# Kernel optimization log

Measured on AMD Instinct MI355X. Metric: run time of the kernel, lower is better.

The kernel has to match this reference:

```python
import jax, jax.numpy as jnp
import numpy as np

K_CONST = 0.005
D_U = 0.001
D_V = 0.005
LAYERS = [3, 256, 256, 256, 256, 2]
N_PTS = 131072


def setup_inputs() -> dict:
    key = jax.random.key(0)
    ks = jax.random.split(key, 3 + 2 * (len(LAYERS) - 1))
    inp = {
        "t": jax.random.uniform(ks[0], (N_PTS, 1), dtype=jnp.float32),
        "x": jax.random.uniform(ks[1], (N_PTS, 1), dtype=jnp.float32),
        "y": jax.random.uniform(ks[2], (N_PTS, 1), dtype=jnp.float32),
    }
    # PyTorch nn.Linear default init: U(-1/sqrt(fan_in), 1/sqrt(fan_in))
    for i in range(len(LAYERS) - 1):
        fan_in = LAYERS[i]
        s = 1.0 / np.sqrt(fan_in)
        inp[f"W{i}"] = jax.random.uniform(ks[3 + 2 * i], (LAYERS[i], LAYERS[i + 1]),
                                          minval=-s, maxval=s, dtype=jnp.float32)
        inp[f"b{i}"] = jax.random.uniform(ks[4 + 2 * i], (LAYERS[i + 1],),
                                          minval=-s, maxval=s, dtype=jnp.float32)
    return inp


def _mlp(params, inp):
    # inp: (3,) -> (2,) tanh MLP (tanh on all but last layer)
    h = inp
    for W, b in params[:-1]:
        h = jnp.tanh(h @ W + b)
    W, b = params[-1]
    return h @ W + b


def reference(t, x, y, W0, b0, W1, b1, W2, b2, W3, b3, W4, b4):
    params = [(W0, b0), (W1, b1), (W2, b2), (W3, b3), (W4, b4)]
    net = lambda p: _mlp(params, p)  # (3,) -> (2,)

    pts = jnp.concatenate([t, x, y], axis=1)            # (N, 3)
    uv = jax.vmap(net)(pts)                              # (N, 2)
    jac = jax.vmap(jax.jacrev(net))(pts)                 # (N, 2, 3)
    hess = jax.vmap(jax.jacfwd(jax.jacrev(net)))(pts)    # (N, 2, 3, 3)

    u = uv[:, 0:1]
    v = uv[:, 1:2]
    u_t = jac[:, 0, 0:1]
    v_t = jac[:, 1, 0:1]
    u_xx = hess[:, 0, 1, 1][:, None]
    u_yy = hess[:, 0, 2, 2][:, None]
    v_xx = hess[:, 1, 1, 1][:, None]
    v_yy = hess[:, 1, 2, 2][:, None]

    f = u - u ** 3 - K_CONST - v + D_U * (u_xx + u_yy) - u_t
    g = u - v + D_V * (v_xx + v_yy) - v_t
    return (u, v, f, g)
```

## Files before the change

kernel.cpp:

```cpp
#include <hip/hip_runtime.h>
#include <math.h>

#define N_PTS   131072
#define K_CONST 0.005f
#define D_U     0.001f
#define D_V     0.005f

typedef unsigned short u16;
typedef unsigned int   u32;
typedef __attribute__((ext_vector_type(8))) _Float16 f16x8;
typedef __attribute__((ext_vector_type(4))) float    f32x4;
typedef __attribute__((ext_vector_type(4))) u16      u16x4;
typedef __attribute__((ext_vector_type(8))) u16      u16x8;
typedef __attribute__((ext_vector_type(2))) u32      u32x2;
typedef __attribute__((ext_vector_type(4))) u32      u32x4;

__device__ __forceinline__ u16 f2h(float x){
    _Float16 h = (_Float16)x;
    return __builtin_bit_cast(u16, h);
}
__device__ __forceinline__ float h2f(u16 h){
    return (float)__builtin_bit_cast(_Float16, h);
}
__device__ __forceinline__ u32 pkrtz(float a, float b){
    return __builtin_bit_cast(u32, __builtin_amdgcn_cvt_pkrtz(a, b));
}
__device__ __forceinline__ u32x2 pk4(float a, float b, float c, float d){
    u32x2 r;
    r.x = pkrtz(a, b);
    r.y = pkrtz(c, d);
    return r;
}
__device__ __forceinline__ u32x4 pk8(const float* v){
    u32x4 r;
    r.x = pkrtz(v[0], v[1]);
    r.y = pkrtz(v[2], v[3]);
    r.z = pkrtz(v[4], v[5]);
    r.w = pkrtz(v[6], v[7]);
    return r;
}

__device__ __forceinline__ float tanh_fast(float z){
    float e = __expf(2.f * z);
    return 1.f - 2.f * __builtin_amdgcn_rcpf(e + 1.f);
}

__global__ void prep_weights(const float* __restrict__ W1, const float* __restrict__ W2,
                             const float* __restrict__ W3, u16* __restrict__ ws)
{
    int gid  = blockIdx.x * 256 + threadIdx.x;
    int lane = gid & 63;
    int nt   = (gid >> 6) & 15;
    int ks   = (gid >> 10) & 7;
    int L    = gid >> 13;
    if (L >= 3) return;
    const float* W = (L == 0) ? W1 : ((L == 1) ? W2 : W3);
    int n  = nt * 16 + (lane & 15);
    int kg = lane >> 4;
    u16 h[8];
    #pragma unroll
    for (int j = 0; j < 8; ++j) {
        int k = ks * 32 + kg * 8 + j;
        h[j] = f2h(W[k * 256 + n]);
    }
    size_t ostore = ((size_t)((L * 16 + nt) * 8 + ks) * 64 + lane) * 8;
    *(u16x8*)&ws[ostore] = *(u16x8*)h;
}


#define KSTEP(KS, WC, WN, P0, P1)                                                          \
  {                                                                                        \
    WN[0] = *(const f16x8*)(P0);                                                           \
    WN[1] = *(const f16x8*)(P1);                                                           \
    int hoff = mbase + ((64 * (KS) + 16 * kg) ^ mxor);                                     \
    f16x8 hv = *(const f16x8*)(Hb + 0 * 8192 + hoff);                                      \
    f16x8 ht = *(const f16x8*)(Hb + 1 * 8192 + hoff);                                      \
    f16x8 hx = *(const f16x8*)(Hb + 2 * 8192 + hoff);                                      \
    f16x8 hy = *(const f16x8*)(Hb + 3 * 8192 + hoff);                                      \
    f16x8 hl = *(const f16x8*)(Hb + 4 * 8192 + hoff);                                      \
    __builtin_amdgcn_s_setprio(1);                                                         \
    _Pragma("unroll")                                                                      \
    for (int nt = 0; nt < 2; ++nt) {                                                       \
      acc[0][nt] = __builtin_amdgcn_mfma_f32_16x16x32_f16(WC[nt], hv, acc[0][nt], 0, 0, 0);\
      acc[1][nt] = __builtin_amdgcn_mfma_f32_16x16x32_f16(WC[nt], ht, acc[1][nt], 0, 0, 0);\
      acc[2][nt] = __builtin_amdgcn_mfma_f32_16x16x32_f16(WC[nt], hx, acc[2][nt], 0, 0, 0);\
      acc[3][nt] = __builtin_amdgcn_mfma_f32_16x16x32_f16(WC[nt], hy, acc[3][nt], 0, 0, 0);\
      acc[4][nt] = __builtin_amdgcn_mfma_f32_16x16x32_f16(WC[nt], hl, acc[4][nt], 0, 0, 0);\
    }                                                                                      \
    __builtin_amdgcn_s_setprio(0);                                                         \
  }

__global__ __launch_bounds__(512, 4)
void pinn_mfma6(const float* __restrict__ t_in, const float* __restrict__ x_in,
                const float* __restrict__ y_in,
                const float* __restrict__ W0, const float* __restrict__ b0,
                const float* __restrict__ b1, const float* __restrict__ b2,
                const float* __restrict__ b3,
                const float* __restrict__ W4, const float* __restrict__ b4,
                const u16* __restrict__ ws,
                float* __restrict__ out)
{
    __shared__ u16 H[5 * 16 * 256];
    char* Hb = (char*)H;

    const int tid  = threadIdx.x;
    const int lane = tid & 63;
    const int wv   = tid >> 6;

    {
        int p = tid & 15, c = tid >> 4;
        int g0 = blockIdx.x * 16 + p;
        float tv = t_in[g0], xv = x_in[g0], yv = y_in[g0];
        int n0 = c * 8;
        float w0[8], w1[8], w2[8], bb[8];
        #pragma unroll
        for (int q = 0; q < 2; ++q) {
            *(float4*)&w0[q*4] = *(const float4*)&W0[0*256 + n0 + q*4];
            *(float4*)&w1[q*4] = *(const float4*)&W0[1*256 + n0 + q*4];
            *(float4*)&w2[q*4] = *(const float4*)&W0[2*256 + n0 + q*4];
            *(float4*)&bb[q*4] = *(const float4*)&b0[n0 + q*4];
        }
        float sv[8], st[8], sx[8], sy[8], sl[8];
        #pragma unroll
        for (int j = 0; j < 8; ++j) {
            float z = tv*w0[j] + xv*w1[j] + yv*w2[j] + bb[j];
            float a = tanh_fast(z);
            float g = 1.f - a*a;
            sv[j] = a;
            st[j] = g * w0[j];
            sx[j] = g * w1[j];
            sy[j] = g * w2[j];
            sl[j] = -2.f * a * g * (w1[j]*w1[j] + w2[j]*w2[j]);
        }
        int off = p * 512 + ((2 * n0) ^ (p << 4));
        *(u32x4*)(Hb + 0*8192 + off) = pk8(sv);
        *(u32x4*)(Hb + 1*8192 + off) = pk8(st);
        *(u32x4*)(Hb + 2*8192 + off) = pk8(sx);
        *(u32x4*)(Hb + 3*8192 + off) = pk8(sy);
        *(u32x4*)(Hb + 4*8192 + off) = pk8(sl);
    }
    __syncthreads();

    const int mrow  = lane & 15;
    const int kg    = lane >> 4;
    const int mxor  = mrow << 4;
    const int mbase = mrow * 512;

    const u16* pW0 = ws + (size_t)(wv * 2) * 4096 + lane * 8;
    const u16* pW1 = pW0 + 4096;

    f16x8 whA[2], whB[2];
    whA[0] = *(const f16x8*)(pW0);
    whA[1] = *(const f16x8*)(pW1);

    #pragma unroll 1
    for (int L = 0; L < 3; ++L) {
        const float* bL = (L == 0) ? b1 : ((L == 1) ? b2 : b3);

        f32x4 acc[5][2];
        #pragma unroll
        for (int s = 0; s < 5; ++s) {
            acc[s][0] = (f32x4){0.f, 0.f, 0.f, 0.f};
            acc[s][1] = (f32x4){0.f, 0.f, 0.f, 0.f};
        }

        const u16* pL0 = pW0 + L * 65536;
        const u16* pL1 = pW1 + L * 65536;
        const int  Ln  = (L < 2) ? (L + 1) : 2;
        const u16* pN0 = pW0 + Ln * 65536;
        const u16* pN1 = pW1 + Ln * 65536;

        KSTEP(0, whA, whB, pL0 + 1*512, pL1 + 1*512);
        KSTEP(1, whB, whA, pL0 + 2*512, pL1 + 2*512);
        KSTEP(2, whA, whB, pL0 + 3*512, pL1 + 3*512);
        KSTEP(3, whB, whA, pL0 + 4*512, pL1 + 4*512);
        KSTEP(4, whA, whB, pL0 + 5*512, pL1 + 5*512);
        KSTEP(5, whB, whA, pL0 + 6*512, pL1 + 6*512);
        KSTEP(6, whA, whB, pL0 + 7*512, pL1 + 7*512);
        KSTEP(7, whB, whA, pN0, pN1);

        __syncthreads();

        #pragma unroll
        for (int nt = 0; nt < 2; ++nt) {
            int nb = (wv * 2 + nt) * 16 + kg * 4;
            float4 bv = *(const float4*)&bL[nb];
            float bva[4] = {bv.x, bv.y, bv.z, bv.w};
            float oa[4], ot[4], ox[4], oy[4], ol[4];
            #pragma unroll
            for (int r = 0; r < 4; ++r) {
                float z0 = acc[0][nt][r] + bva[r];
                float a  = tanh_fast(z0);
                float g  = 1.f - a * a;
                float zt = acc[1][nt][r];
                float zx = acc[2][nt][r];
                float zy = acc[3][nt][r];
                float zl = acc[4][nt][r];
                oa[r] = a;
                ot[r] = g * zt;
                ox[r] = g * zx;
                oy[r] = g * zy;
                ol[r] = g * zl - 2.f * a * g * (zx*zx + zy*zy);
            }
            int off = mbase + ((2 * nb) ^ mxor);
            *(u32x2*)(Hb + 0*8192 + off) = pk4(oa[0], oa[1], oa[2], oa[3]);
            *(u32x2*)(Hb + 1*8192 + off) = pk4(ot[0], ot[1], ot[2], ot[3]);
            *(u32x2*)(Hb + 2*8192 + off) = pk4(ox[0], ox[1], ox[2], ox[3]);
            *(u32x2*)(Hb + 3*8192 + off) = pk4(oy[0], oy[1], oy[2], oy[3]);
            *(u32x2*)(Hb + 4*8192 + off) = pk4(ol[0], ol[1], ol[2], ol[3]);
        }
        __syncthreads();
    }

    {
        int p = tid >> 5, i = tid & 31;
        int k0 = i * 8;
        int off = p * 512 + ((2 * k0) ^ (p << 4));
        u16x8 hv = *(const u16x8*)(Hb + 0*8192 + off);
        u16x8 ht = *(const u16x8*)(Hb + 1*8192 + off);
        u16x8 hl = *(const u16x8*)(Hb + 4*8192 + off);
        float w4[16];
        #pragma unroll
        for (int q = 0; q < 4; ++q)
            *(float4*)&w4[q*4] = *(const float4*)&W4[k0 * 2 + q * 4];
        float pu = 0.f, pv = 0.f, put = 0.f, pvt = 0.f, plu = 0.f, plv = 0.f;
        #pragma unroll
        for (int j = 0; j < 8; ++j) {
            float vv = h2f(hv[j]);
            float tt = h2f(ht[j]);
            float ll = h2f(hl[j]);
            float wa = w4[2*j], wb2 = w4[2*j + 1];
            pu  += vv * wa;  pv  += vv * wb2;
            put += tt * wa;  pvt += tt * wb2;
            plu += ll * wa;  plv += ll * wb2;
        }
        #pragma unroll
        for (int m = 1; m < 32; m <<= 1) {
            pu  += __shfl_xor(pu, m);   pv  += __shfl_xor(pv, m);
            put += __shfl_xor(put, m);  pvt += __shfl_xor(pvt, m);
            plu += __shfl_xor(plu, m);  plv += __shfl_xor(plv, m);
        }
        if (i == 0) {
            float u = pu + b4[0];
            float v = pv + b4[1];
            int gpt = blockIdx.x * 16 + p;
            float fo = u - u*u*u - K_CONST - v + D_U * plu - put;
            float go = u - v + D_V * plv - pvt;
            out[0 * N_PTS + gpt] = u;
            out[1 * N_PTS + gpt] = v;
            out[2 * N_PTS + gpt] = fo;
            out[3 * N_PTS + gpt] = go;
        }
    }
}

#define PTS   16
#define NTHR  256
#define HDIM  256
#define KC    32
#define HPAD  260

__global__ __launch_bounds__(NTHR, 1)
void pinn_diffreact_f32(const float* __restrict__ t_in, const float* __restrict__ x_in,
                        const float* __restrict__ y_in,
                        const float* __restrict__ W0, const float* __restrict__ b0,
                        const float* __restrict__ W1, const float* __restrict__ b1,
                        const float* __restrict__ W2, const float* __restrict__ b2,
                        const float* __restrict__ W3, const float* __restrict__ b3,
                        const float* __restrict__ W4, const float* __restrict__ b4,
                        float* __restrict__ out)
{
    __shared__ float Hs[6 * PTS * HPAD];
    __shared__ float Wc[KC * HDIM];
    const int tid = threadIdx.x;
    const int pt = tid >> 4;
    const int fbase = (tid & 15) * 4;
    const int gpt = blockIdx.x * PTS + pt;
    {
        const float tv = t_in[gpt], xv = x_in[gpt], yv = y_in[gpt];
        #pragma unroll
        for (int jv = 0; jv < 4; ++jv)
            #pragma unroll
            for (int q = 0; q < 4; ++q) {
                const int f = fbase + jv * 64 + q;
                const float w0 = W0[f], w1 = W0[256 + f], w2 = W0[512 + f];
                const float z = tv*w0 + xv*w1 + yv*w2 + b0[f];
                const float a = tanhf(z), g = 1.f - a*a;
                Hs[(0*PTS+pt)*HPAD+f] = a;
                Hs[(1*PTS+pt)*HPAD+f] = g*w0;
                Hs[(2*PTS+pt)*HPAD+f] = g*w1;
                Hs[(3*PTS+pt)*HPAD+f] = g*w2;
                Hs[(4*PTS+pt)*HPAD+f] = -2.f*a*g*w1*w1;
                Hs[(5*PTS+pt)*HPAD+f] = -2.f*a*g*w2*w2;
            }
    }
    __syncthreads();
    const float* Ws[3] = {W1, W2, W3};
    const float* bs[3] = {b1, b2, b3};
    for (int L = 0; L < 3; ++L) {
        const float* __restrict__ W = Ws[L];
        const float* __restrict__ b = bs[L];
        float acc[6][16];
        #pragma unroll
        for (int s = 0; s < 6; ++s)
            #pragma unroll
            for (int j = 0; j < 16; ++j) acc[s][j] = 0.f;
        for (int kc = 0; kc < HDIM / KC; ++kc) {
            __syncthreads();
            const float4* src = (const float4*)(W + kc * KC * HDIM);
            float4* dst = (float4*)Wc;
            #pragma unroll
            for (int i2 = 0; i2 < (KC * HDIM / 4) / NTHR; ++i2)
                dst[tid + i2 * NTHR] = src[tid + i2 * NTHR];
            __syncthreads();
            #pragma unroll
            for (int k4 = 0; k4 < KC; k4 += 4) {
                float4 h[6];
                #pragma unroll
                for (int s = 0; s < 6; ++s)
                    h[s] = *(const float4*)&Hs[(s*PTS+pt)*HPAD + kc*KC + k4];
                #pragma unroll
                for (int q = 0; q < 4; ++q) {
                    float hv[6];
                    #pragma unroll
                    for (int s = 0; s < 6; ++s)
                        hv[s] = (q==0) ? h[s].x : (q==1) ? h[s].y : (q==2) ? h[s].z : h[s].w;
                    #pragma unroll
                    for (int jv = 0; jv < 4; ++jv) {
                        const float4 wq = *(const float4*)&Wc[(k4+q)*HDIM + fbase + jv*64];
                        const float wvv[4] = {wq.x, wq.y, wq.z, wq.w};
                        #pragma unroll
                        for (int r = 0; r < 4; ++r)
                            #pragma unroll
                            for (int s = 0; s < 6; ++s)
                                acc[s][jv*4+r] += hv[s] * wvv[r];
                    }
                }
            }
        }
        __syncthreads();
        #pragma unroll
        for (int jv = 0; jv < 4; ++jv)
            #pragma unroll
            for (int q = 0; q < 4; ++q) {
                const int j = jv*4+q, f = fbase + jv*64 + q;
                const float z = acc[0][j] + b[f];
                const float a = tanhf(z), g = 1.f - a*a;
                const float zt = acc[1][j], zx = acc[2][j], zy = acc[3][j];
                const float zxx = acc[4][j], zyy = acc[5][j];
                Hs[(0*PTS+pt)*HPAD+f] = a;
                Hs[(1*PTS+pt)*HPAD+f] = g*zt;
                Hs[(2*PTS+pt)*HPAD+f] = g*zx;
                Hs[(3*PTS+pt)*HPAD+f] = g*zy;
                Hs[(4*PTS+pt)*HPAD+f] = g*zxx - 2.f*a*g*zx*zx;
                Hs[(5*PTS+pt)*HPAD+f] = g*zyy - 2.f*a*g*zy*zy;
            }
        __syncthreads();
    }
    float p[6][2];
    #pragma unroll
    for (int s = 0; s < 6; ++s) { p[s][0] = 0.f; p[s][1] = 0.f; }
    #pragma unroll
    for (int jv = 0; jv < 4; ++jv)
        #pragma unroll
        for (int q = 0; q < 4; ++q) {
            const int f = fbase + jv*64 + q;
            const float w0 = W4[f*2], w1 = W4[f*2+1];
            #pragma unroll
            for (int s = 0; s < 6; ++s) {
                const float hv = Hs[(s*PTS+pt)*HPAD+f];
                p[s][0] += hv*w0; p[s][1] += hv*w1;
            }
        }
    #pragma unroll
    for (int m = 1; m < 16; m <<= 1)
        #pragma unroll
        for (int s = 0; s < 6; ++s) {
            p[s][0] += __shfl_xor(p[s][0], m);
            p[s][1] += __shfl_xor(p[s][1], m);
        }
    if ((tid & 15) == 0) {
        const float u = p[0][0] + b4[0];
        const float v = p[0][1] + b4[1];
        const float ut = p[1][0], vt = p[1][1];
        const float uxx = p[4][0], vxx = p[4][1];
        const float uyy = p[5][0], vyy = p[5][1];
        const float fo = u - u*u*u - K_CONST - v + D_U*(uxx+uyy) - ut;
        const float go = u - v + D_V*(vxx+vyy) - vt;
        out[0*N_PTS+gpt] = u;
        out[1*N_PTS+gpt] = v;
        out[2*N_PTS+gpt] = fo;
        out[3*N_PTS+gpt] = go;
    }
}

extern "C" void kernel_launch(void* const* d_in, const int* in_sizes, int n_in,
                              void* d_out, int out_size, void* d_ws, size_t ws_size,
                              hipStream_t stream)
{
    const float* t_in = (const float*)d_in[0];
    const float* x_in = (const float*)d_in[1];
    const float* y_in = (const float*)d_in[2];
    const float* W0 = (const float*)d_in[3];
    const float* b0 = (const float*)d_in[4];
    const float* W1 = (const float*)d_in[5];
    const float* b1 = (const float*)d_in[6];
    const float* W2 = (const float*)d_in[7];
    const float* b2 = (const float*)d_in[8];
    const float* W3 = (const float*)d_in[9];
    const float* b3 = (const float*)d_in[10];
    const float* W4 = (const float*)d_in[11];
    const float* b4 = (const float*)d_in[12];
    float* out = (float*)d_out;

    const size_t WS_NEEDED = (size_t)3 * 8 * 16 * 64 * 8 * 2;
    if (ws_size >= WS_NEEDED) {
        u16* ws = (u16*)d_ws;
        hipLaunchKernelGGL(prep_weights, dim3(96), dim3(256), 0, stream, W1, W2, W3, ws);
        hipLaunchKernelGGL(pinn_mfma6, dim3(N_PTS / 16), dim3(512), 0, stream,
                           t_in, x_in, y_in, W0, b0, b1, b2, b3, W4, b4, ws, out);
    } else {
        hipLaunchKernelGGL(pinn_diffreact_f32, dim3(N_PTS / PTS), dim3(NTHR), 0, stream,
                           t_in, x_in, y_in, W0, b0, W1, b1, W2, b2, W3, b3, W4, b4, out);
    }
}
```

Measured before the change: 291.6 us.

## Switch hidden-layer MFMA to 32x32x16 tiles with 32 points per block

Replaces the 16x16x32 MFMA tiling with 32x32x16 instructions, processing 32 points per block with 4 waves, each owning 64 output columns. The weight pre-pack layout, the LDS buffer size and swizzle, the epilogue indexing and the final reduction are all reworked for the new fragment shapes. The aim is more arithmetic per weight fragment loaded and higher MFMA throughput per instruction. In exchange, each thread holds many more accumulator registers (160 floats), which may limit occupancy or cause spills.

```diff
diff --git a/kernel.cpp b/kernel.cpp
--- a/kernel.cpp
+++ b/kernel.cpp
@@ -8,12 +8,12 @@
 
 typedef unsigned short u16;
 typedef unsigned int   u32;
-typedef __attribute__((ext_vector_type(8))) _Float16 f16x8;
-typedef __attribute__((ext_vector_type(4))) float    f32x4;
-typedef __attribute__((ext_vector_type(4))) u16      u16x4;
-typedef __attribute__((ext_vector_type(8))) u16      u16x8;
-typedef __attribute__((ext_vector_type(2))) u32      u32x2;
-typedef __attribute__((ext_vector_type(4))) u32      u32x4;
+typedef __attribute__((ext_vector_type(8)))  _Float16 f16x8;
+typedef __attribute__((ext_vector_type(16))) float    f32x16;
+typedef __attribute__((ext_vector_type(4)))  u16      u16x4;
+typedef __attribute__((ext_vector_type(8)))  u16      u16x8;
+typedef __attribute__((ext_vector_type(2)))  u32      u32x2;
+typedef __attribute__((ext_vector_type(4)))  u32      u32x4;
 
 __device__ __forceinline__ u16 f2h(float x){
     _Float16 h = (_Float16)x;
@@ -26,72 +26,66 @@
     return __builtin_bit_cast(u32, __builtin_amdgcn_cvt_pkrtz(a, b));
 }
 __device__ __forceinline__ u32x2 pk4(float a, float b, float c, float d){
-    u32x2 r;
-    r.x = pkrtz(a, b);
-    r.y = pkrtz(c, d);
-    return r;
+    u32x2 r; r.x = pkrtz(a, b); r.y = pkrtz(c, d); return r;
 }
 __device__ __forceinline__ u32x4 pk8(const float* v){
     u32x4 r;
-    r.x = pkrtz(v[0], v[1]);
-    r.y = pkrtz(v[2], v[3]);
-    r.z = pkrtz(v[4], v[5]);
-    r.w = pkrtz(v[6], v[7]);
+    r.x = pkrtz(v[0], v[1]); r.y = pkrtz(v[2], v[3]);
+    r.z = pkrtz(v[4], v[5]); r.w = pkrtz(v[6], v[7]);
     return r;
 }
-
 __device__ __forceinline__ float tanh_fast(float z){
     float e = __expf(2.f * z);
     return 1.f - 2.f * __builtin_amdgcn_rcpf(e + 1.f);
 }
 
-__global__ void prep_weights(const float* __restrict__ W1, const float* __restrict__ W2,
-                             const float* __restrict__ W3, u16* __restrict__ ws)
+__global__ void prep_weights32(const float* __restrict__ W1, const float* __restrict__ W2,
+                               const float* __restrict__ W3, u16* __restrict__ ws)
 {
     int gid  = blockIdx.x * 256 + threadIdx.x;
     int lane = gid & 63;
-    int nt   = (gid >> 6) & 15;
-    int ks   = (gid >> 10) & 7;
+    int ks   = (gid >> 6) & 15;
+    int nt   = (gid >> 10) & 7;
     int L    = gid >> 13;
     if (L >= 3) return;
     const float* W = (L == 0) ? W1 : ((L == 1) ? W2 : W3);
-    int n  = nt * 16 + (lane & 15);
-    int kg = lane >> 4;
+    int n  = nt * 32 + (lane & 31);
+    int kg = lane >> 5;
     u16 h[8];
     #pragma unroll
     for (int j = 0; j < 8; ++j) {
-        int k = ks * 32 + kg * 8 + j;
+        int k = ks * 16 + kg * 8 + j;
         h[j] = f2h(W[k * 256 + n]);
     }
-    size_t ostore = ((size_t)((L * 16 + nt) * 8 + ks) * 64 + lane) * 8;
+    size_t ostore = ((size_t)((L * 8 + nt) * 16 + ks) * 64 + lane) * 8;
     *(u16x8*)&ws[ostore] = *(u16x8*)h;
 }
 
 
-#define KSTEP(KS, WC, WN, P0, P1)                                                          \
-  {                                                                                        \
-    WN[0] = *(const f16x8*)(P0);                                                           \
-    WN[1] = *(const f16x8*)(P1);                                                           \
-    int hoff = mbase + ((64 * (KS) + 16 * kg) ^ mxor);                                     \
-    f16x8 hv = *(const f16x8*)(Hb + 0 * 8192 + hoff);                                      \
-    f16x8 ht = *(const f16x8*)(Hb + 1 * 8192 + hoff);                                      \
-    f16x8 hx = *(const f16x8*)(Hb + 2 * 8192 + hoff);                                      \
-    f16x8 hy = *(const f16x8*)(Hb + 3 * 8192 + hoff);                                      \
-    f16x8 hl = *(const f16x8*)(Hb + 4 * 8192 + hoff);                                      \
-    __builtin_amdgcn_s_setprio(1);                                                         \
-    _Pragma("unroll")                                                                      \
-    for (int nt = 0; nt < 2; ++nt) {                                                       \
-      acc[0][nt] = __builtin_amdgcn_mfma_f32_16x16x32_f16(WC[nt], hv, acc[0][nt], 0, 0, 0);\
-      acc[1][nt] = __builtin_amdgcn_mfma_f32_16x16x32_f16(WC[nt], ht, acc[1][nt], 0, 0, 0);\
-      acc[2][nt] = __builtin_amdgcn_mfma_f32_16x16x32_f16(WC[nt], hx, acc[2][nt], 0, 0, 0);\
-      acc[3][nt] = __builtin_amdgcn_mfma_f32_16x16x32_f16(WC[nt], hy, acc[3][nt], 0, 0, 0);\
-      acc[4][nt] = __builtin_amdgcn_mfma_f32_16x16x32_f16(WC[nt], hl, acc[4][nt], 0, 0, 0);\
-    }                                                                                      \
-    __builtin_amdgcn_s_setprio(0);                                                         \
+#define KSTEP(KS, WC, WN, P0, P1, O)                                                           \
+  {                                                                                            \
+    WN[0] = *(const f16x8*)((P0) + (O));                                                       \
+    WN[1] = *(const f16x8*)((P1) + (O));                                                       \
+    int hoff = mbase + ((32 * (KS) + kh16) ^ mxor);                                            \
+    f16x8 hv = *(const f16x8*)(Hb + 0 * 16384 + hoff);                                         \
+    f16x8 ht = *(const f16x8*)(Hb + 1 * 16384 + hoff);                                         \
+    f16x8 hx = *(const f16x8*)(Hb + 2 * 16384 + hoff);                                         \
+    f16x8 hy = *(const f16x8*)(Hb + 3 * 16384 + hoff);                                         \
+    f16x8 hl = *(const f16x8*)(Hb + 4 * 16384 + hoff);                                         \
+    __builtin_amdgcn_s_setprio(1);                                                             \
+    _Pragma("unroll")                                                                          \
+    for (int nt = 0; nt < 2; ++nt) {                                                           \
+      acc[0][nt] = __builtin_amdgcn_mfma_f32_32x32x16_f16(WC[nt], hv, acc[0][nt], 0, 0, 0);    \
+      acc[1][nt] = __builtin_amdgcn_mfma_f32_32x32x16_f16(WC[nt], ht, acc[1][nt], 0, 0, 0);    \
+      acc[2][nt] = __builtin_amdgcn_mfma_f32_32x32x16_f16(WC[nt], hx, acc[2][nt], 0, 0, 0);    \
+      acc[3][nt] = __builtin_amdgcn_mfma_f32_32x32x16_f16(WC[nt], hy, acc[3][nt], 0, 0, 0);    \
+      acc[4][nt] = __builtin_amdgcn_mfma_f32_32x32x16_f16(WC[nt], hl, acc[4][nt], 0, 0, 0);    \
+    }                                                                                          \
+    __builtin_amdgcn_s_setprio(0);                                                             \
   }
 
-__global__ __launch_bounds__(512, 4)
-void pinn_mfma6(const float* __restrict__ t_in, const float* __restrict__ x_in,
+__global__ __launch_bounds__(256, 2)
+void pinn_mfma9(const float* __restrict__ t_in, const float* __restrict__ x_in,
                 const float* __restrict__ y_in,
                 const float* __restrict__ W0, const float* __restrict__ b0,
                 const float* __restrict__ b1, const float* __restrict__ b2,
@@ -100,7 +94,7 @@
                 const u16* __restrict__ ws,
                 float* __restrict__ out)
 {
-    __shared__ u16 H[5 * 16 * 256];
+    __shared__ u16 H[5 * 32 * 256];
     char* Hb = (char*)H;
 
     const int tid  = threadIdx.x;
@@ -108,46 +102,50 @@
     const int wv   = tid >> 6;
 
     {
-        int p = tid & 15, c = tid >> 4;
-        int g0 = blockIdx.x * 16 + p;
+        int p = tid & 31, c = tid >> 5;
+        int g0 = blockIdx.x * 32 + p;
         float tv = t_in[g0], xv = x_in[g0], yv = y_in[g0];
-        int n0 = c * 8;
-        float w0[8], w1[8], w2[8], bb[8];
-        #pragma unroll
-        for (int q = 0; q < 2; ++q) {
-            *(float4*)&w0[q*4] = *(const float4*)&W0[0*256 + n0 + q*4];
-            *(float4*)&w1[q*4] = *(const float4*)&W0[1*256 + n0 + q*4];
-            *(float4*)&w2[q*4] = *(const float4*)&W0[2*256 + n0 + q*4];
-            *(float4*)&bb[q*4] = *(const float4*)&b0[n0 + q*4];
-        }
-        float sv[8], st[8], sx[8], sy[8], sl[8];
-        #pragma unroll
-        for (int j = 0; j < 8; ++j) {
-            float z = tv*w0[j] + xv*w1[j] + yv*w2[j] + bb[j];
-            float a = tanh_fast(z);
-            float g = 1.f - a*a;
-            sv[j] = a;
-            st[j] = g * w0[j];
-            sx[j] = g * w1[j];
-            sy[j] = g * w2[j];
-            sl[j] = -2.f * a * g * (w1[j]*w1[j] + w2[j]*w2[j]);
-        }
-        int off = p * 512 + ((2 * n0) ^ (p << 4));
-        *(u32x4*)(Hb + 0*8192 + off) = pk8(sv);
-        *(u32x4*)(Hb + 1*8192 + off) = pk8(st);
-        *(u32x4*)(Hb + 2*8192 + off) = pk8(sx);
-        *(u32x4*)(Hb + 3*8192 + off) = pk8(sy);
-        *(u32x4*)(Hb + 4*8192 + off) = pk8(sl);
+        #pragma unroll
+        for (int cc = 0; cc < 4; ++cc) {
+            int n0 = c * 32 + cc * 8;
+            float w0[8], w1[8], w2[8], bb[8];
+            #pragma unroll
+            for (int q = 0; q < 2; ++q) {
+                *(float4*)&w0[q*4] = *(const float4*)&W0[0*256 + n0 + q*4];
+                *(float4*)&w1[q*4] = *(const float4*)&W0[1*256 + n0 + q*4];
+                *(float4*)&w2[q*4] = *(const float4*)&W0[2*256 + n0 + q*4];
+                *(float4*)&bb[q*4] = *(const float4*)&b0[n0 + q*4];
+            }
+            float sv[8], st[8], sx[8], sy[8], sl[8];
+            #pragma unroll
+            for (int j = 0; j < 8; ++j) {
+                float z = tv*w0[j] + xv*w1[j] + yv*w2[j] + bb[j];
+                float a = tanh_fast(z);
+                float g = 1.f - a*a;
+                sv[j] = a;
+                st[j] = g * w0[j];
+                sx[j] = g * w1[j];
+                sy[j] = g * w2[j];
+                sl[j] = -2.f * a * g * (w1[j]*w1[j] + w2[j]*w2[j]);
+            }
+            int off = p * 512 + ((2 * n0) ^ ((p & 15) << 4));
+            *(u32x4*)(Hb + 0*16384 + off) = pk8(sv);
+            *(u32x4*)(Hb + 1*16384 + off) = pk8(st);
+            *(u32x4*)(Hb + 2*16384 + off) = pk8(sx);
+            *(u32x4*)(Hb + 3*16384 + off) = pk8(sy);
+            *(u32x4*)(Hb + 4*16384 + off) = pk8(sl);
+        }
     }
     __syncthreads();
 
-    const int mrow  = lane & 15;
-    const int kg    = lane >> 4;
-    const int mxor  = mrow << 4;
-    const int mbase = mrow * 512;
-
-    const u16* pW0 = ws + (size_t)(wv * 2) * 4096 + lane * 8;
-    const u16* pW1 = pW0 + 4096;
+    const int prow  = lane & 31;
+    const int kh16  = (lane >> 5) * 16;
+    const int mxor  = (prow & 15) << 4;
+    const int mbase = prow * 512;
+    const int rbase = (lane >> 5) * 4;
+
+    const u16* pW0 = ws + (size_t)(wv * 2) * 8192 + lane * 8;
+    const u16* pW1 = pW0 + 8192;
 
     f16x8 whA[2], whB[2];
     whA[0] = *(const f16x8*)(pW0);
@@ -157,11 +155,14 @@
     for (int L = 0; L < 3; ++L) {
         const float* bL = (L == 0) ? b1 : ((L == 1) ? b2 : b3);
 
-        f32x4 acc[5][2];
+        f32x16 acc[5][2];
         #pragma unroll
         for (int s = 0; s < 5; ++s) {
-            acc[s][0] = (f32x4){0.f, 0.f, 0.f, 0.f};
-            acc[s][1] = (f32x4){0.f, 0.f, 0.f, 0.f};
+            #pragma unroll
+            for (int nt = 0; nt < 2; ++nt)
+                #pragma unroll
+                for (int r = 0; r < 16; ++r)
+                    acc[s][nt][r] = 0.f;
         }
 
         const u16* pL0 = pW0 + L * 65536;
@@ -170,72 +171,87 @@
         const u16* pN0 = pW0 + Ln * 65536;
         const u16* pN1 = pW1 + Ln * 65536;
 
-        KSTEP(0, whA, whB, pL0 + 1*512, pL1 + 1*512);
-        KSTEP(1, whB, whA, pL0 + 2*512, pL1 + 2*512);
-        KSTEP(2, whA, whB, pL0 + 3*512, pL1 + 3*512);
-        KSTEP(3, whB, whA, pL0 + 4*512, pL1 + 4*512);
-        KSTEP(4, whA, whB, pL0 + 5*512, pL1 + 5*512);
-        KSTEP(5, whB, whA, pL0 + 6*512, pL1 + 6*512);
-        KSTEP(6, whA, whB, pL0 + 7*512, pL1 + 7*512);
-        KSTEP(7, whB, whA, pN0, pN1);
+        KSTEP( 0, whA, whB, pL0, pL1,  1*512);
+        KSTEP( 1, whB, whA, pL0, pL1,  2*512);
+        KSTEP( 2, whA, whB, pL0, pL1,  3*512);
+        KSTEP( 3, whB, whA, pL0, pL1,  4*512);
+        KSTEP( 4, whA, whB, pL0, pL1,  5*512);
+        KSTEP( 5, whB, whA, pL0, pL1,  6*512);
+        KSTEP( 6, whA, whB, pL0, pL1,  7*512);
+        KSTEP( 7, whB, whA, pL0, pL1,  8*512);
+        KSTEP( 8, whA, whB, pL0, pL1,  9*512);
+        KSTEP( 9, whB, whA, pL0, pL1, 10*512);
+        KSTEP(10, whA, whB, pL0, pL1, 11*512);
+        KSTEP(11, whB, whA, pL0, pL1, 12*512);
+        KSTEP(12, whA, whB, pL0, pL1, 13*512);
+        KSTEP(13, whB, whA, pL0, pL1, 14*512);
+        KSTEP(14, whA, whB, pL0, pL1, 15*512);
+        KSTEP(15, whB, whA, pN0, pN1, 0);
 
         __syncthreads();
 
         #pragma unroll
         for (int nt = 0; nt < 2; ++nt) {
-            int nb = (wv * 2 + nt) * 16 + kg * 4;
-            float4 bv = *(const float4*)&bL[nb];
-            float bva[4] = {bv.x, bv.y, bv.z, bv.w};
-            float oa[4], ot[4], ox[4], oy[4], ol[4];
-            #pragma unroll
-            for (int r = 0; r < 4; ++r) {
-                float z0 = acc[0][nt][r] + bva[r];
-                float a  = tanh_fast(z0);
-                float g  = 1.f - a * a;
-                float zt = acc[1][nt][r];
-                float zx = acc[2][nt][r];
-                float zy = acc[3][nt][r];
-                float zl = acc[4][nt][r];
-                oa[r] = a;
-                ot[r] = g * zt;
-                ox[r] = g * zx;
-                oy[r] = g * zy;
-                ol[r] = g * zl - 2.f * a * g * (zx*zx + zy*zy);
-            }
-            int off = mbase + ((2 * nb) ^ mxor);
-            *(u32x2*)(Hb + 0*8192 + off) = pk4(oa[0], oa[1], oa[2], oa[3]);
-            *(u32x2*)(Hb + 1*8192 + off) = pk4(ot[0], ot[1], ot[2], ot[3]);
-            *(u32x2*)(Hb + 2*8192 + off) = pk4(ox[0], ox[1], ox[2], ox[3]);
-            *(u32x2*)(Hb + 3*8192 + off) = pk4(oy[0], oy[1], oy[2], oy[3]);
-            *(u32x2*)(Hb + 4*8192 + off) = pk4(ol[0], ol[1], ol[2], ol[3]);
+            int ntb = (wv * 2 + nt) * 32;
+            #pragma unroll
+            for (int q = 0; q < 4; ++q) {
+                int n0q = ntb + 8 * q + rbase;
+                float4 bv = *(const float4*)&bL[n0q];
+                float bva[4] = {bv.x, bv.y, bv.z, bv.w};
+                float oa[4], ot[4], ox[4], oy[4], ol[4];
+                #pragma unroll
+                for (int r = 0; r < 4; ++r) {
+                    float z0 = acc[0][nt][4*q + r] + bva[r];
+                    float a  = tanh_fast(z0);
+                    float g  = 1.f - a * a;
+                    float zt = acc[1][nt][4*q + r];
+                    float zx = acc[2][nt][4*q + r];
+                    float zy = acc[3][nt][4*q + r];
+                    float zl = acc[4][nt][4*q + r];
+                    oa[r] = a;
+                    ot[r] = g * zt;
+                    ox[r] = g * zx;
+                    oy[r] = g * zy;
+                    ol[r] = g * zl - 2.f * a * g * (zx*zx + zy*zy);
+                }
+                int off = mbase + ((2 * n0q) ^ mxor);
+                *(u32x2*)(Hb + 0*16384 + off) = pk4(oa[0], oa[1], oa[2], oa[3]);
+                *(u32x2*)(Hb + 1*16384 + off) = pk4(ot[0], ot[1], ot[2], ot[3]);
+                *(u32x2*)(Hb + 2*16384 + off) = pk4(ox[0], ox[1], ox[2], ox[3]);
+                *(u32x2*)(Hb + 3*16384 + off) = pk4(oy[0], oy[1], oy[2], oy[3]);
+                *(u32x2*)(Hb + 4*16384 + off) = pk4(ol[0], ol[1], ol[2], ol[3]);
+            }
         }
         __syncthreads();
     }
 
     {
-        int p = tid >> 5, i = tid & 31;
-        int k0 = i * 8;
-        int off = p * 512 + ((2 * k0) ^ (p << 4));
-        u16x8 hv = *(const u16x8*)(Hb + 0*8192 + off);
-        u16x8 ht = *(const u16x8*)(Hb + 1*8192 + off);
-        u16x8 hl = *(const u16x8*)(Hb + 4*8192 + off);
-        float w4[16];
-        #pragma unroll
-        for (int q = 0; q < 4; ++q)
-            *(float4*)&w4[q*4] = *(const float4*)&W4[k0 * 2 + q * 4];
+        int p = tid >> 3, i = tid & 7;
         float pu = 0.f, pv = 0.f, put = 0.f, pvt = 0.f, plu = 0.f, plv = 0.f;
         #pragma unroll
-        for (int j = 0; j < 8; ++j) {
-            float vv = h2f(hv[j]);
-            float tt = h2f(ht[j]);
-            float ll = h2f(hl[j]);
-            float wa = w4[2*j], wb2 = w4[2*j + 1];
-            pu  += vv * wa;  pv  += vv * wb2;
-            put += tt * wa;  pvt += tt * wb2;
-            plu += ll * wa;  plv += ll * wb2;
-        }
-        #pragma unroll
-        for (int m = 1; m < 32; m <<= 1) {
+        for (int cc = 0; cc < 4; ++cc) {
+            int k0  = i * 32 + cc * 8;
+            int off = p * 512 + ((2 * k0) ^ ((p & 15) << 4));
+            u16x8 hv = *(const u16x8*)(Hb + 0*16384 + off);
+            u16x8 ht = *(const u16x8*)(Hb + 1*16384 + off);
+            u16x8 hl = *(const u16x8*)(Hb + 4*16384 + off);
+            float w4[16];
+            #pragma unroll
+            for (int q = 0; q < 4; ++q)
+                *(float4*)&w4[q*4] = *(const float4*)&W4[k0 * 2 + q * 4];
+            #pragma unroll
+            for (int j = 0; j < 8; ++j) {
+                float vv = h2f(hv[j]);
+                float tt = h2f(ht[j]);
+                float ll = h2f(hl[j]);
+                float wa = w4[2*j], wb2 = w4[2*j + 1];
+                pu  += vv * wa;  pv  += vv * wb2;
+                put += tt * wa;  pvt += tt * wb2;
+                plu += ll * wa;  plv += ll * wb2;
+            }
+        }
+        #pragma unroll
+        for (int m = 1; m < 8; m <<= 1) {
             pu  += __shfl_xor(pu, m);   pv  += __shfl_xor(pv, m);
             put += __shfl_xor(put, m);  pvt += __shfl_xor(pvt, m);
             plu += __shfl_xor(plu, m);  plv += __shfl_xor(plv, m);
@@ -243,7 +259,7 @@
         if (i == 0) {
             float u = pu + b4[0];
             float v = pv + b4[1];
-            int gpt = blockIdx.x * 16 + p;
+            int gpt = blockIdx.x * 32 + p;
             float fo = u - u*u*u - K_CONST - v + D_U * plu - put;
             float go = u - v + D_V * plv - pvt;
             out[0 * N_PTS + gpt] = u;
@@ -413,11 +429,11 @@
     const float* b4 = (const float*)d_in[12];
     float* out = (float*)d_out;
 
-    const size_t WS_NEEDED = (size_t)3 * 8 * 16 * 64 * 8 * 2;
+    const size_t WS_NEEDED = (size_t)3 * 65536 * 2;
     if (ws_size >= WS_NEEDED) {
         u16* ws = (u16*)d_ws;
-        hipLaunchKernelGGL(prep_weights, dim3(96), dim3(256), 0, stream, W1, W2, W3, ws);
-        hipLaunchKernelGGL(pinn_mfma6, dim3(N_PTS / 16), dim3(512), 0, stream,
+        hipLaunchKernelGGL(prep_weights32, dim3(96), dim3(256), 0, stream, W1, W2, W3, ws);
+        hipLaunchKernelGGL(pinn_mfma9, dim3(N_PTS / 32), dim3(256), 0, stream,
                            t_in, x_in, y_in, W0, b0, b1, b2, b3, W4, b4, ws, out);
     } else {
         hipLaunchKernelGGL(pinn_diffreact_f32, dim3(N_PTS / PTS), dim3(NTHR), 0, stream,
```

Result: faster. 279.4 us, median of 2 (-4.2%).

## Use 4 waves per block with 4 N-tiles each instead of 8 waves

Applied to the files above, without the earlier changes.

Halves the block size from 512 to 256 threads, so each wave computes four 16-column output tiles per layer instead of two. This doubles the accumulators and weight registers per wave and reuses each LDS activation fragment across more MFMAs. The next-layer weight prefetch moves after the last k-step, and the setprio hints are removed. In exchange it raises register pressure, lowers wave count per block, and changes the launch bounds to (256,3), which may cut occupancy.

```diff
diff --git a/kernel.cpp b/kernel.cpp
--- a/kernel.cpp
+++ b/kernel.cpp
@@ -26,20 +26,14 @@
     return __builtin_bit_cast(u32, __builtin_amdgcn_cvt_pkrtz(a, b));
 }
 __device__ __forceinline__ u32x2 pk4(float a, float b, float c, float d){
-    u32x2 r;
-    r.x = pkrtz(a, b);
-    r.y = pkrtz(c, d);
-    return r;
+    u32x2 r; r.x = pkrtz(a, b); r.y = pkrtz(c, d); return r;
 }
 __device__ __forceinline__ u32x4 pk8(const float* v){
     u32x4 r;
-    r.x = pkrtz(v[0], v[1]);
-    r.y = pkrtz(v[2], v[3]);
-    r.z = pkrtz(v[4], v[5]);
-    r.w = pkrtz(v[6], v[7]);
+    r.x = pkrtz(v[0], v[1]); r.y = pkrtz(v[2], v[3]);
+    r.z = pkrtz(v[4], v[5]); r.w = pkrtz(v[6], v[7]);
     return r;
 }
-
 __device__ __forceinline__ float tanh_fast(float z){
     float e = __expf(2.f * z);
     return 1.f - 2.f * __builtin_amdgcn_rcpf(e + 1.f);
@@ -68,37 +62,55 @@
 }
 
 
-#define KSTEP(KS, WC, WN, P0, P1)                                                          \
+#define KSTEP(KS, WC, WN, PN, O)                                                           \
   {                                                                                        \
-    WN[0] = *(const f16x8*)(P0);                                                           \
-    WN[1] = *(const f16x8*)(P1);                                                           \
+    WN[0] = *(const f16x8*)((PN) + 0 * 4096 + (O));                                        \
+    WN[1] = *(const f16x8*)((PN) + 1 * 4096 + (O));                                        \
+    WN[2] = *(const f16x8*)((PN) + 2 * 4096 + (O));                                        \
+    WN[3] = *(const f16x8*)((PN) + 3 * 4096 + (O));                                        \
     int hoff = mbase + ((64 * (KS) + 16 * kg) ^ mxor);                                     \
     f16x8 hv = *(const f16x8*)(Hb + 0 * 8192 + hoff);                                      \
     f16x8 ht = *(const f16x8*)(Hb + 1 * 8192 + hoff);                                      \
     f16x8 hx = *(const f16x8*)(Hb + 2 * 8192 + hoff);                                      \
     f16x8 hy = *(const f16x8*)(Hb + 3 * 8192 + hoff);                                      \
     f16x8 hl = *(const f16x8*)(Hb + 4 * 8192 + hoff);                                      \
-    __builtin_amdgcn_s_setprio(1);                                                         \
     _Pragma("unroll")                                                                      \
-    for (int nt = 0; nt < 2; ++nt) {                                                       \
+    for (int nt = 0; nt < 4; ++nt) {                                                       \
       acc[0][nt] = __builtin_amdgcn_mfma_f32_16x16x32_f16(WC[nt], hv, acc[0][nt], 0, 0, 0);\
       acc[1][nt] = __builtin_amdgcn_mfma_f32_16x16x32_f16(WC[nt], ht, acc[1][nt], 0, 0, 0);\
       acc[2][nt] = __builtin_amdgcn_mfma_f32_16x16x32_f16(WC[nt], hx, acc[2][nt], 0, 0, 0);\
       acc[3][nt] = __builtin_amdgcn_mfma_f32_16x16x32_f16(WC[nt], hy, acc[3][nt], 0, 0, 0);\
       acc[4][nt] = __builtin_amdgcn_mfma_f32_16x16x32_f16(WC[nt], hl, acc[4][nt], 0, 0, 0);\
     }                                                                                      \
-    __builtin_amdgcn_s_setprio(0);                                                         \
   }
 
-__global__ __launch_bounds__(512, 4)
-void pinn_mfma6(const float* __restrict__ t_in, const float* __restrict__ x_in,
-                const float* __restrict__ y_in,
-                const float* __restrict__ W0, const float* __restrict__ b0,
-                const float* __restrict__ b1, const float* __restrict__ b2,
-                const float* __restrict__ b3,
-                const float* __restrict__ W4, const float* __restrict__ b4,
-                const u16* __restrict__ ws,
-                float* __restrict__ out)
+#define KSTEP7(WC)                                                                         \
+  {                                                                                        \
+    int hoff = mbase + ((64 * 7 + 16 * kg) ^ mxor);                                        \
+    f16x8 hv = *(const f16x8*)(Hb + 0 * 8192 + hoff);                                      \
+    f16x8 ht = *(const f16x8*)(Hb + 1 * 8192 + hoff);                                      \
+    f16x8 hx = *(const f16x8*)(Hb + 2 * 8192 + hoff);                                      \
+    f16x8 hy = *(const f16x8*)(Hb + 3 * 8192 + hoff);                                      \
+    f16x8 hl = *(const f16x8*)(Hb + 4 * 8192 + hoff);                                      \
+    _Pragma("unroll")                                                                      \
+    for (int nt = 0; nt < 4; ++nt) {                                                       \
+      acc[0][nt] = __builtin_amdgcn_mfma_f32_16x16x32_f16(WC[nt], hv, acc[0][nt], 0, 0, 0);\
+      acc[1][nt] = __builtin_amdgcn_mfma_f32_16x16x32_f16(WC[nt], ht, acc[1][nt], 0, 0, 0);\
+      acc[2][nt] = __builtin_amdgcn_mfma_f32_16x16x32_f16(WC[nt], hx, acc[2][nt], 0, 0, 0);\
+      acc[3][nt] = __builtin_amdgcn_mfma_f32_16x16x32_f16(WC[nt], hy, acc[3][nt], 0, 0, 0);\
+      acc[4][nt] = __builtin_amdgcn_mfma_f32_16x16x32_f16(WC[nt], hl, acc[4][nt], 0, 0, 0);\
+    }                                                                                      \
+  }
+
+__global__ __launch_bounds__(256, 3)
+void pinn_mfma10(const float* __restrict__ t_in, const float* __restrict__ x_in,
+                 const float* __restrict__ y_in,
+                 const float* __restrict__ W0, const float* __restrict__ b0,
+                 const float* __restrict__ b1, const float* __restrict__ b2,
+                 const float* __restrict__ b3,
+                 const float* __restrict__ W4, const float* __restrict__ b4,
+                 const u16* __restrict__ ws,
+                 float* __restrict__ out)
 {
     __shared__ u16 H[5 * 16 * 256];
     char* Hb = (char*)H;
@@ -111,33 +123,36 @@
         int p = tid & 15, c = tid >> 4;
         int g0 = blockIdx.x * 16 + p;
         float tv = t_in[g0], xv = x_in[g0], yv = y_in[g0];
-        int n0 = c * 8;
-        float w0[8], w1[8], w2[8], bb[8];
-        #pragma unroll
-        for (int q = 0; q < 2; ++q) {
-            *(float4*)&w0[q*4] = *(const float4*)&W0[0*256 + n0 + q*4];
-            *(float4*)&w1[q*4] = *(const float4*)&W0[1*256 + n0 + q*4];
-            *(float4*)&w2[q*4] = *(const float4*)&W0[2*256 + n0 + q*4];
-            *(float4*)&bb[q*4] = *(const float4*)&b0[n0 + q*4];
-        }
-        float sv[8], st[8], sx[8], sy[8], sl[8];
-        #pragma unroll
-        for (int j = 0; j < 8; ++j) {
-            float z = tv*w0[j] + xv*w1[j] + yv*w2[j] + bb[j];
-            float a = tanh_fast(z);
-            float g = 1.f - a*a;
-            sv[j] = a;
-            st[j] = g * w0[j];
-            sx[j] = g * w1[j];
-            sy[j] = g * w2[j];
-            sl[j] = -2.f * a * g * (w1[j]*w1[j] + w2[j]*w2[j]);
-        }
-        int off = p * 512 + ((2 * n0) ^ (p << 4));
-        *(u32x4*)(Hb + 0*8192 + off) = pk8(sv);
-        *(u32x4*)(Hb + 1*8192 + off) = pk8(st);
-        *(u32x4*)(Hb + 2*8192 + off) = pk8(sx);
-        *(u32x4*)(Hb + 3*8192 + off) = pk8(sy);
-        *(u32x4*)(Hb + 4*8192 + off) = pk8(sl);
+        #pragma unroll
+        for (int half = 0; half < 2; ++half) {
+            int n0 = c * 16 + half * 8;
+            float w0[8], w1[8], w2[8], bb[8];
+            #pragma unroll
+            for (int q = 0; q < 2; ++q) {
+                *(float4*)&w0[q*4] = *(const float4*)&W0[0*256 + n0 + q*4];
+                *(float4*)&w1[q*4] = *(const float4*)&W0[1*256 + n0 + q*4];
+                *(float4*)&w2[q*4] = *(const float4*)&W0[2*256 + n0 + q*4];
+                *(float4*)&bb[q*4] = *(const float4*)&b0[n0 + q*4];
+            }
+            float sv[8], st[8], sx[8], sy[8], sl[8];
+            #pragma unroll
+            for (int j = 0; j < 8; ++j) {
+                float z = tv*w0[j] + xv*w1[j] + yv*w2[j] + bb[j];
+                float a = tanh_fast(z);
+                float g = 1.f - a*a;
+                sv[j] = a;
+                st[j] = g * w0[j];
+                sx[j] = g * w1[j];
+                sy[j] = g * w2[j];
+                sl[j] = -2.f * a * g * (w1[j]*w1[j] + w2[j]*w2[j]);
+            }
+            int off = p * 512 + ((2 * n0) ^ (p << 4));
+            *(u32x4*)(Hb + 0*8192 + off) = pk8(sv);
+            *(u32x4*)(Hb + 1*8192 + off) = pk8(st);
+            *(u32x4*)(Hb + 2*8192 + off) = pk8(sx);
+            *(u32x4*)(Hb + 3*8192 + off) = pk8(sy);
+            *(u32x4*)(Hb + 4*8192 + off) = pk8(sl);
+        }
     }
     __syncthreads();
 
@@ -146,44 +161,46 @@
     const int mxor  = mrow << 4;
     const int mbase = mrow * 512;
 
-    const u16* pW0 = ws + (size_t)(wv * 2) * 4096 + lane * 8;
-    const u16* pW1 = pW0 + 4096;
-
-    f16x8 whA[2], whB[2];
-    whA[0] = *(const f16x8*)(pW0);
-    whA[1] = *(const f16x8*)(pW1);
+    const u16* pWb = ws + (size_t)(wv * 4) * 4096 + lane * 8;
+
+    f16x8 whA[4], whB[4];
+    #pragma unroll
+    for (int nt = 0; nt < 4; ++nt)
+        whA[nt] = *(const f16x8*)(pWb + nt * 4096);
 
     #pragma unroll 1
     for (int L = 0; L < 3; ++L) {
         const float* bL = (L == 0) ? b1 : ((L == 1) ? b2 : b3);
 
-        f32x4 acc[5][2];
-        #pragma unroll
-        for (int s = 0; s < 5; ++s) {
-            acc[s][0] = (f32x4){0.f, 0.f, 0.f, 0.f};
-            acc[s][1] = (f32x4){0.f, 0.f, 0.f, 0.f};
-        }
-
-        const u16* pL0 = pW0 + L * 65536;
-        const u16* pL1 = pW1 + L * 65536;
-        const int  Ln  = (L < 2) ? (L + 1) : 2;
-        const u16* pN0 = pW0 + Ln * 65536;
-        const u16* pN1 = pW1 + Ln * 65536;
-
-        KSTEP(0, whA, whB, pL0 + 1*512, pL1 + 1*512);
-        KSTEP(1, whB, whA, pL0 + 2*512, pL1 + 2*512);
-        KSTEP(2, whA, whB, pL0 + 3*512, pL1 + 3*512);
-        KSTEP(3, whB, whA, pL0 + 4*512, pL1 + 4*512);
-        KSTEP(4, whA, whB, pL0 + 5*512, pL1 + 5*512);
-        KSTEP(5, whB, whA, pL0 + 6*512, pL1 + 6*512);
-        KSTEP(6, whA, whB, pL0 + 7*512, pL1 + 7*512);
-        KSTEP(7, whB, whA, pN0, pN1);
+        f32x4 acc[5][4];
+        #pragma unroll
+        for (int s = 0; s < 5; ++s)
+            #pragma unroll
+            for (int nt = 0; nt < 4; ++nt)
+                acc[s][nt] = (f32x4){0.f, 0.f, 0.f, 0.f};
+
+        const u16* pL = pWb + L * 65536;
+        const int  Ln = (L < 2) ? (L + 1) : 2;
+        const u16* pN = pWb + Ln * 65536;
+
+        KSTEP(0, whA, whB, pL, 1*512);
+        KSTEP(1, whB, whA, pL, 2*512);
+        KSTEP(2, whA, whB, pL, 3*512);
+        KSTEP(3, whB, whA, pL, 4*512);
+        KSTEP(4, whA, whB, pL, 5*512);
+        KSTEP(5, whB, whA, pL, 6*512);
+        KSTEP(6, whA, whB, pL, 7*512);
+        KSTEP7(whB);
+
+        #pragma unroll
+        for (int nt = 0; nt < 4; ++nt)
+            whA[nt] = *(const f16x8*)(pN + nt * 4096);
 
         __syncthreads();
 
         #pragma unroll
-        for (int nt = 0; nt < 2; ++nt) {
-            int nb = (wv * 2 + nt) * 16 + kg * 4;
+        for (int nt = 0; nt < 4; ++nt) {
+            int nb = (wv * 4 + nt) * 16 + kg * 4;
             float4 bv = *(const float4*)&bL[nb];
             float bva[4] = {bv.x, bv.y, bv.z, bv.w};
             float oa[4], ot[4], ox[4], oy[4], ol[4];
@@ -213,29 +230,32 @@
     }
 
     {
-        int p = tid >> 5, i = tid & 31;
-        int k0 = i * 8;
-        int off = p * 512 + ((2 * k0) ^ (p << 4));
-        u16x8 hv = *(const u16x8*)(Hb + 0*8192 + off);
-        u16x8 ht = *(const u16x8*)(Hb + 1*8192 + off);
-        u16x8 hl = *(const u16x8*)(Hb + 4*8192 + off);
-        float w4[16];
-        #pragma unroll
-        for (int q = 0; q < 4; ++q)
-            *(float4*)&w4[q*4] = *(const float4*)&W4[k0 * 2 + q * 4];
+        int p = tid >> 4, i = tid & 15;
         float pu = 0.f, pv = 0.f, put = 0.f, pvt = 0.f, plu = 0.f, plv = 0.f;
         #pragma unroll
-        for (int j = 0; j < 8; ++j) {
-            float vv = h2f(hv[j]);
-            float tt = h2f(ht[j]);
-            float ll = h2f(hl[j]);
-            float wa = w4[2*j], wb2 = w4[2*j + 1];
-            pu  += vv * wa;  pv  += vv * wb2;
-            put += tt * wa;  pvt += tt * wb2;
-            plu += ll * wa;  plv += ll * wb2;
-        }
-        #pragma unroll
-        for (int m = 1; m < 32; m <<= 1) {
+        for (int half = 0; half < 2; ++half) {
+            int k0  = i * 16 + half * 8;
+            int off = p * 512 + ((2 * k0) ^ (p << 4));
+            u16x8 hv = *(const u16x8*)(Hb + 0*8192 + off);
+            u16x8 ht = *(const u16x8*)(Hb + 1*8192 + off);
+            u16x8 hl = *(const u16x8*)(Hb + 4*8192 + off);
+            float w4[16];
+            #pragma unroll
+            for (int q = 0; q < 4; ++q)
+                *(float4*)&w4[q*4] = *(const float4*)&W4[k0 * 2 + q * 4];
+            #pragma unroll
+            for (int j = 0; j < 8; ++j) {
+                float vv = h2f(hv[j]);
+                float tt = h2f(ht[j]);
+                float ll = h2f(hl[j]);
+                float wa = w4[2*j], wb2 = w4[2*j + 1];
+                pu  += vv * wa;  pv  += vv * wb2;
+                put += tt * wa;  pvt += tt * wb2;
+                plu += ll * wa;  plv += ll * wb2;
+            }
+        }
+        #pragma unroll
+        for (int m = 1; m < 16; m <<= 1) {
             pu  += __shfl_xor(pu, m);   pv  += __shfl_xor(pv, m);
             put += __shfl_xor(put, m);  pvt += __shfl_xor(pvt, m);
             plu += __shfl_xor(plu, m);  plv += __shfl_xor(plv, m);
@@ -413,11 +433,11 @@
     const float* b4 = (const float*)d_in[12];
     float* out = (float*)d_out;
 
-    const size_t WS_NEEDED = (size_t)3 * 8 * 16 * 64 * 8 * 2;
+    const size_t WS_NEEDED = (size_t)3 * 16 * 8 * 64 * 8 * 2;
     if (ws_size >= WS_NEEDED) {
         u16* ws = (u16*)d_ws;
         hipLaunchKernelGGL(prep_weights, dim3(96), dim3(256), 0, stream, W1, W2, W3, ws);
-        hipLaunchKernelGGL(pinn_mfma6, dim3(N_PTS / 16), dim3(512), 0, stream,
+        hipLaunchKernelGGL(pinn_mfma10, dim3(N_PTS / 16), dim3(256), 0, stream,
                            t_in, x_in, y_in, W0, b0, b1, b2, b3, W4, b4, ws, out);
     } else {
         hipLaunchKernelGGL(pinn_diffreact_f32, dim3(N_PTS / PTS), dim3(NTHR), 0, stream,
```

After: 297.5 us. 1.02x slower.
